# Kernel tuning notes

Measured on AMD Instinct MI355X. Metric: run time of the kernel, lower is better.

## Reference

```python
import jax, jax.numpy as jnp
import numpy as np

MIN_VAL = 1e-12  # Ln(min_val=1e-12) in MorphLayer
KSIZE = 3
STRIDE = 1


def _patches(x, k, s):
    # x: (B, C, H, W) -> (B, C*k*k, Ho, Wo), im2col like torch unfold
    return jax.lax.conv_general_dilated_patches(x, (k, k), (s, s), 'VALID')


def _max_plus(p, w):
    # log-domain morphological conv: (B, K, Ho, Wo) + (K, F) -> max over K -> (B, F, Ho, Wo)
    return jnp.max(p[:, :, None, :, :] + w[None, :, :, None, None], axis=1)


def setup_inputs() -> dict:
    key = jax.random.key(0)
    k1, k2, k3 = jax.random.split(key, 3)
    B, C, H, W = 16, 3, 66, 66
    F = 32
    K = C * KSIZE * KSIZE  # 27
    return {
        'x': jax.random.normal(k1, (B, C, H, W), dtype=jnp.float32),
        'kernel_k1': jax.random.normal(k2, (K, F), dtype=jnp.float32) * 0.1,
        'kernel_k2': jax.random.normal(k3, (K, F), dtype=jnp.float32) * 0.1,
        'bias': jnp.zeros((F,), dtype=jnp.float32),
    }


def reference(x, kernel_k1, kernel_k2, bias):
    # Ln: log of positive / negative parts, clamped at MIN_VAL
    x1 = jnp.log(jnp.maximum(x, MIN_VAL))
    x2 = jnp.log(jnp.maximum(-x, MIN_VAL))
    p1 = _patches(x1, KSIZE, STRIDE)  # (B, K, Ho, Wo)
    p2 = _patches(x2, KSIZE, STRIDE)
    y11 = jnp.exp(_max_plus(p1, kernel_k1))
    y12 = jnp.exp(_max_plus(p1, kernel_k2))
    y21 = jnp.exp(_max_plus(p2, kernel_k1))
    y22 = jnp.exp(_max_plus(p2, kernel_k2))
    return y11 - y12 - y21 + y22 + bias[None, :, None, None]
```

## Files before the change

### kernel.cpp

```cpp
#include <hip/hip_runtime.h>
#include <math.h>


#define BB 16
#define CC 3
#define HH 66
#define WW 66
#define HO 64
#define WO 64
#define FF 32
#define KK 27
#define FPG 4
#define FG (FF / FPG)
#define ROWS 4
#define IR (ROWS + 2)

typedef float f32x2 __attribute__((ext_vector_type(2)));

__global__ __launch_bounds__(256, 8)
void morph_fused(const float* __restrict__ x,
                 const float* __restrict__ k1,
                 const float* __restrict__ k2,
                 const float* __restrict__ bias,
                 float* __restrict__ out) {
    __shared__ float xs[CC * IR * WW];
    __shared__ float wl[KK * 8];

    const int tid = threadIdx.x;
    int bid = blockIdx.x;
    const int fg = bid & (FG - 1); bid >>= 3;
    const int rg = bid & 15;       bid >>= 4;
    const int b  = bid;
    const int f0 = fg * FPG;
    const int ho0 = rg * ROWS;

    if (tid < KK * 8) {
        const int k = tid >> 3;
        const int j = tid & 3;
        const int h = (tid >> 2) & 1;
        const float w = h ? k2[k * FF + f0 + j] : k1[k * FF + f0 + j];
        wl[tid] = expf(w);
    }
    const float* xb = x + (size_t)b * CC * HH * WW;
    for (int i = tid; i < CC * IR * WW; i += 256) {
        const int c   = i / (IR * WW);
        const int rem = i - c * (IR * WW);
        const int row = rem / WW;
        const int col = rem - row * WW;
        xs[i] = xb[(c * HH + ho0 + row) * WW + col];
    }
    __syncthreads();

    const int wo = tid & 63;
    const int r  = tid >> 6;
    const int ho = ho0 + r;

    float m11x = 0.f, m11y = 0.f, m11z = 0.f, m11w = 0.f;
    float m12x = 0.f, m12y = 0.f, m12z = 0.f, m12w = 0.f;
    float m21x = 0.f, m21y = 0.f, m21z = 0.f, m21w = 0.f;
    float m22x = 0.f, m22y = 0.f, m22z = 0.f, m22w = 0.f;

    const f32x2* wl2 = (const f32x2*)wl;

    #pragma unroll
    for (int c = 0; c < CC; ++c) {
        #pragma unroll
        for (int di = 0; di < 3; ++di) {
            #pragma unroll
            for (int dj = 0; dj < 3; ++dj) {
                const int k = c * 9 + di * 3 + dj;
                const float v = xs[(c * IR + r + di) * WW + wo + dj];
                const f32x2 vv = {v, v};
                const f32x2 p1a = vv * wl2[k * 4 + 0];
                const f32x2 p1b = vv * wl2[k * 4 + 1];
                const f32x2 p2a = vv * wl2[k * 4 + 2];
                const f32x2 p2b = vv * wl2[k * 4 + 3];
                m11x = fmaxf(m11x, p1a.x);  m11y = fmaxf(m11y, p1a.y);
                m11z = fmaxf(m11z, p1b.x);  m11w = fmaxf(m11w, p1b.y);
                m12x = fmaxf(m12x, p2a.x);  m12y = fmaxf(m12y, p2a.y);
                m12z = fmaxf(m12z, p2b.x);  m12w = fmaxf(m12w, p2b.y);
                m21x = fmaxf(m21x, -p1a.x); m21y = fmaxf(m21y, -p1a.y);
                m21z = fmaxf(m21z, -p1b.x); m21w = fmaxf(m21w, -p1b.y);
                m22x = fmaxf(m22x, -p2a.x); m22y = fmaxf(m22y, -p2a.y);
                m22z = fmaxf(m22z, -p2b.x); m22w = fmaxf(m22w, -p2b.y);
            }
        }
    }

    const size_t obase = ((size_t)b * FF + f0) * (HO * WO) + (size_t)ho * WO + wo;
    out[obase + 0 * HO * WO] = m11x - m12x - m21x + m22x + bias[f0 + 0];
    out[obase + 1 * HO * WO] = m11y - m12y - m21y + m22y + bias[f0 + 1];
    out[obase + 2 * HO * WO] = m11z - m12z - m21z + m22z + bias[f0 + 2];
    out[obase + 3 * HO * WO] = m11w - m12w - m21w + m22w + bias[f0 + 3];
}

extern "C" void kernel_launch(void* const* d_in, const int* in_sizes, int n_in,
                              void* d_out, int out_size, void* d_ws, size_t ws_size,
                              hipStream_t stream) {
    const float* x    = (const float*)d_in[0];
    const float* k1   = (const float*)d_in[1];
    const float* k2   = (const float*)d_in[2];
    const float* bias = (const float*)d_in[3];
    float* out = (float*)d_out;

    const int nblocks = BB * (HO / ROWS) * FG;
    morph_fused<<<dim3(nblocks), dim3(256), 0, stream>>>(x, k1, k2, bias, out);
}
```

Baseline: 13.88 us.

## Remap threads to one filter per wave with 4 output columns each

Each wave now handles a single output filter and each thread computes four adjacent output columns instead of four filters at one pixel. Input rows are read from a padded shared buffer as vector loads and reused across the three horizontal taps, which cuts LDS reads per output. Outputs are written as float4 stores. Weight loads become per-wave broadcasts.

```diff
diff --git a/kernel.cpp b/kernel.cpp
--- a/kernel.cpp
+++ b/kernel.cpp
@@ -10,88 +10,105 @@
 #define WO 64
 #define FF 32
 #define KK 27
-#define FPG 4
-#define FG (FF / FPG)
+#define FPB 4
+#define FG (FF / FPB)
 #define ROWS 4
 #define IR (ROWS + 2)
+#define LP 68
+#define WSTRIDE 56
 
 typedef float f32x2 __attribute__((ext_vector_type(2)));
+typedef float f32x4 __attribute__((ext_vector_type(4)));
 
 __global__ __launch_bounds__(256, 8)
-void morph_fused(const float* __restrict__ x,
-                 const float* __restrict__ k1,
-                 const float* __restrict__ k2,
-                 const float* __restrict__ bias,
-                 float* __restrict__ out) {
-    __shared__ float xs[CC * IR * WW];
-    __shared__ float wl[KK * 8];
+void morph_tile(const float* __restrict__ x,
+                const float* __restrict__ k1,
+                const float* __restrict__ k2,
+                const float* __restrict__ bias,
+                float* __restrict__ out) {
+    __shared__ __align__(16) float xs[CC * IR * LP];
+    __shared__ __align__(16) float wl[FPB * WSTRIDE];
 
     const int tid = threadIdx.x;
     int bid = blockIdx.x;
     const int fg = bid & (FG - 1); bid >>= 3;
-    const int rg = bid & 15;       bid >>= 4;
+    const int rb = bid & 15;       bid >>= 4;
     const int b  = bid;
-    const int f0 = fg * FPG;
-    const int ho0 = rg * ROWS;
+    const int f0 = fg * FPB;
+    const int ho0 = rb * ROWS;
 
-    if (tid < KK * 8) {
-        const int k = tid >> 3;
-        const int j = tid & 3;
-        const int h = (tid >> 2) & 1;
-        const float w = h ? k2[k * FF + f0 + j] : k1[k * FF + f0 + j];
-        wl[tid] = expf(w);
+    if (tid < FPB * KK * 2) {
+        const int w_  = tid / (KK * 2);
+        const int rem = tid - w_ * (KK * 2);
+        const int k   = rem >> 1;
+        const int h   = rem & 1;
+        const float wv = h ? k2[k * FF + f0 + w_] : k1[k * FF + f0 + w_];
+        wl[w_ * WSTRIDE + k * 2 + h] = expf(wv);
     }
-    const float* xb = x + (size_t)b * CC * HH * WW;
+    const float* xbase = x + (size_t)b * CC * HH * WW;
     for (int i = tid; i < CC * IR * WW; i += 256) {
         const int c   = i / (IR * WW);
         const int rem = i - c * (IR * WW);
         const int row = rem / WW;
         const int col = rem - row * WW;
-        xs[i] = xb[(c * HH + ho0 + row) * WW + col];
+        xs[(c * IR + row) * LP + col] = xbase[(c * HH + ho0 + row) * WW + col];
     }
     __syncthreads();
 
-    const int wo = tid & 63;
-    const int r  = tid >> 6;
-    const int ho = ho0 + r;
+    const int w   = tid >> 6;
+    const int l   = tid & 63;
+    const int rr  = l >> 4;
+    const int wo4 = (l & 15) * 4;
 
-    float m11x = 0.f, m11y = 0.f, m11z = 0.f, m11w = 0.f;
-    float m12x = 0.f, m12y = 0.f, m12z = 0.f, m12w = 0.f;
-    float m21x = 0.f, m21y = 0.f, m21z = 0.f, m21w = 0.f;
-    float m22x = 0.f, m22y = 0.f, m22z = 0.f, m22w = 0.f;
+    const float* wlw = wl + w * WSTRIDE;
+    const int f = f0 + w;
 
-    const f32x2* wl2 = (const f32x2*)wl;
+    float m11_0 = 0.f, m11_1 = 0.f, m11_2 = 0.f, m11_3 = 0.f;
+    float m12_0 = 0.f, m12_1 = 0.f, m12_2 = 0.f, m12_3 = 0.f;
+    float m21_0 = 0.f, m21_1 = 0.f, m21_2 = 0.f, m21_3 = 0.f;
+    float m22_0 = 0.f, m22_1 = 0.f, m22_2 = 0.f, m22_3 = 0.f;
 
-    #pragma unroll
-    for (int c = 0; c < CC; ++c) {
-        #pragma unroll
-        for (int di = 0; di < 3; ++di) {
-            #pragma unroll
-            for (int dj = 0; dj < 3; ++dj) {
-                const int k = c * 9 + di * 3 + dj;
-                const float v = xs[(c * IR + r + di) * WW + wo + dj];
-                const f32x2 vv = {v, v};
-                const f32x2 p1a = vv * wl2[k * 4 + 0];
-                const f32x2 p1b = vv * wl2[k * 4 + 1];
-                const f32x2 p2a = vv * wl2[k * 4 + 2];
-                const f32x2 p2b = vv * wl2[k * 4 + 3];
-                m11x = fmaxf(m11x, p1a.x);  m11y = fmaxf(m11y, p1a.y);
-                m11z = fmaxf(m11z, p1b.x);  m11w = fmaxf(m11w, p1b.y);
-                m12x = fmaxf(m12x, p2a.x);  m12y = fmaxf(m12y, p2a.y);
-                m12z = fmaxf(m12z, p2b.x);  m12w = fmaxf(m12w, p2b.y);
-                m21x = fmaxf(m21x, -p1a.x); m21y = fmaxf(m21y, -p1a.y);
-                m21z = fmaxf(m21z, -p1b.x); m21w = fmaxf(m21w, -p1b.y);
-                m22x = fmaxf(m22x, -p2a.x); m22y = fmaxf(m22y, -p2a.y);
-                m22z = fmaxf(m22z, -p2b.x); m22w = fmaxf(m22w, -p2b.y);
-            }
-        }
+#define TAP(k, va, vb, vc, vd) { \
+        const f32x2 e = *(const f32x2*)(wlw + (k) * 2);   \
+        const f32x2 ab = {va, vb}, cd = {vc, vd}; \
+        const f32x2 e1 = {e.x, e.x}, e2 = {e.y, e.y}; \
+        const f32x2 p1 = ab * e1, q1 = cd * e1; \
+        const f32x2 p2 = ab * e2, q2 = cd * e2; \
+        m11_0 = fmaxf(m11_0,  p1.x); m11_1 = fmaxf(m11_1,  p1.y); \
+        m11_2 = fmaxf(m11_2,  q1.x); m11_3 = fmaxf(m11_3,  q1.y); \
+        m12_0 = fmaxf(m12_0,  p2.x); m12_1 = fmaxf(m12_1,  p2.y); \
+        m12_2 = fmaxf(m12_2,  q2.x); m12_3 = fmaxf(m12_3,  q2.y); \
+        m21_0 = fmaxf(m21_0, -p1.x); m21_1 = fmaxf(m21_1, -p1.y); \
+        m21_2 = fmaxf(m21_2, -q1.x); m21_3 = fmaxf(m21_3, -q1.y); \
+        m22_0 = fmaxf(m22_0, -p2.x); m22_1 = fmaxf(m22_1, -p2.y); \
+        m22_2 = fmaxf(m22_2, -q2.x); m22_3 = fmaxf(m22_3, -q2.y); \
     }
 
-    const size_t obase = ((size_t)b * FF + f0) * (HO * WO) + (size_t)ho * WO + wo;
-    out[obase + 0 * HO * WO] = m11x - m12x - m21x + m22x + bias[f0 + 0];
-    out[obase + 1 * HO * WO] = m11y - m12y - m21y + m22y + bias[f0 + 1];
-    out[obase + 2 * HO * WO] = m11z - m12z - m21z + m22z + bias[f0 + 2];
-    out[obase + 3 * HO * WO] = m11w - m12w - m21w + m22w + bias[f0 + 3];
+#define CHUNK(c, di) { \
+        const int base_ = ((c * IR + rr + (di)) * LP + wo4); \
+        const f32x4 xq = *(const f32x4*)(xs + base_); \
+        const f32x2 xr = *(const f32x2*)(xs + base_ + 4); \
+        const float s0 = xq.x, s1 = xq.y, s2 = xq.z, s3 = xq.w; \
+        const float s4 = xr.x, s5 = xr.y; \
+        TAP((c) * 9 + (di) * 3 + 0, s0, s1, s2, s3) \
+        TAP((c) * 9 + (di) * 3 + 1, s1, s2, s3, s4) \
+        TAP((c) * 9 + (di) * 3 + 2, s2, s3, s4, s5) \
+    }
+
+    CHUNK(0, 0) CHUNK(0, 1) CHUNK(0, 2)
+    CHUNK(1, 0) CHUNK(1, 1) CHUNK(1, 2)
+    CHUNK(2, 0) CHUNK(2, 1) CHUNK(2, 2)
+#undef CHUNK
+#undef TAP
+
+    const float bs = bias[f];
+    f32x4 res;
+    res.x = m11_0 - m12_0 - m21_0 + m22_0 + bs;
+    res.y = m11_1 - m12_1 - m21_1 + m22_1 + bs;
+    res.z = m11_2 - m12_2 - m21_2 + m22_2 + bs;
+    res.w = m11_3 - m12_3 - m21_3 + m22_3 + bs;
+
+    *(f32x4*)(out + (((size_t)b * FF + f) * HO + ho0 + rr) * WO + wo4) = res;
 }
 
 extern "C" void kernel_launch(void* const* d_in, const int* in_sizes, int n_in,
@@ -104,5 +121,5 @@
     float* out = (float*)d_out;
 
     const int nblocks = BB * (HO / ROWS) * FG;
-    morph_fused<<<dim3(nblocks), dim3(256), 0, stream>>>(x, k1, k2, bias, out);
+    morph_tile<<<dim3(nblocks), dim3(256), 0, stream>>>(x, k1, k2, bias, out);
 }
```

Measured after the change: 14.73 us. +6.1%, slower.
